# Optimization experiments

Measured on AMD Instinct MI355X. Metric: run time of the kernel, lower is better.

The kernel has to match this reference:

```python
import jax, jax.numpy as jnp
import numpy as np


def setup_inputs() -> dict:
    key = jax.random.key(0)
    k1, k2 = jax.random.split(key)
    return {
        "embeddings": jax.random.normal(k1, (4, 768, 32, 32), dtype=jnp.float32),
        "database": jax.random.normal(k2, (20000, 768), dtype=jnp.float32),
        "k": 3,
        "out_h": 512,
        "out_w": 512,
    }


def reference(embeddings, database, k, out_h, out_w):
    # embeddings: [B, D, h, w]  (segmenter hidden state), database: [N, D]
    B, D, h, w = embeddings.shape
    # B x h x w x D -> B x (h*w) x D query layout, as in _get_ood_scores
    q = jnp.transpose(embeddings, (0, 2, 3, 1)).reshape(B, h * w, D)
    # squared Euclidean distances via (||q||^2 + ||x||^2 - 2 q.x)
    q2 = jnp.sum(q * q, axis=-1)[..., None]                 # [B, hw, 1]
    x2 = jnp.sum(database * database, axis=-1)[None, None]  # [1, 1, N]
    d2 = q2 + x2 - 2.0 * jnp.einsum("bqd,nd->bqn", q, database)
    dist = jnp.sqrt(jnp.maximum(d2, 1e-12))                 # [B, hw, N]
    # k smallest distances (sklearn kneighbors) then mean over neighbors
    neg_topk, _ = jax.lax.top_k(-dist, k)                   # [B, hw, k]
    ood = jnp.mean(-neg_topk, axis=-1).reshape(B, h, w)
    # F.interpolate(..., mode='bilinear', align_corners=False) == half-pixel bilinear
    ood_up = jax.image.resize(ood[:, None], (B, 1, out_h, out_w), method="bilinear")
    return ood_up
```

## Files before the change

### kernel.cpp

```cpp
#include <hip/hip_runtime.h>
#include <hip/hip_bf16.h>
#include <math.h>

constexpr int B    = 4;
constexpr int D    = 768;
constexpr int HW   = 1024;
constexpr int M    = B * HW;
constexpr int NDB  = 20000;
constexpr int LT   = 158;
constexpr int OUTH = 512;
constexpr int OUTW = 512;

constexpr int BM     = 256;
constexpr int BN     = 128;
constexpr int KSTEPS = D / 64;
constexpr int NSPLIT = 16;
constexpr int NT2    = 79;
constexpr int STEPB  = 128 * 64;

typedef int   i32x8  __attribute__((ext_vector_type(8)));
typedef float f32x16 __attribute__((ext_vector_type(16)));

__device__ __forceinline__ void insert3(float& t0, float& t1, float& t2, float d) {
    float a0 = fminf(d, t0);
    float b0 = fmaxf(d, t0);
    float a1 = fminf(b0, t1);
    float b1 = fmaxf(b0, t1);
    t0 = a0; t1 = a1;
    t2 = fminf(b1, t2);
}

__device__ __forceinline__ unsigned int pack4_fp8(float a, float b, float c, float d) {
    int v = __builtin_amdgcn_cvt_pk_fp8_f32(a, b, 0, false);
    v = __builtin_amdgcn_cvt_pk_fp8_f32(c, d, v, true);
    return (unsigned int)v;
}

__device__ __forceinline__ void gl_lds16(const unsigned char* g, unsigned char* l) {
    __builtin_amdgcn_global_load_lds(
        (const __attribute__((address_space(1))) void*)g,
        (__attribute__((address_space(3))) void*)l, 16, 0, 0);
}

__global__ __launch_bounds__(256) void convert_all(const float* __restrict__ db,
                                                   const float* __restrict__ emb,
                                                   uint4* __restrict__ dbt8,
                                                   uint4* __restrict__ qbt8,
                                                   float* __restrict__ x2p,
                                                   float* __restrict__ q2p) {
    __shared__ float panel[128][68];
    __shared__ float part[512];
    const int g = blockIdx.y;
    const int t = threadIdx.x;

    if (blockIdx.x < LT) {
        const int lt = blockIdx.x;
        const int n0 = lt * 128;

        #pragma unroll
        for (int pass = 0; pass < 8; ++pass) {
            int idx = pass * 256 + t;
            int row = idx >> 4, c4 = idx & 15;
            int n = n0 + row;
            float4 v = make_float4(0.f, 0.f, 0.f, 0.f);
            if (n < NDB) v = *(const float4*)(db + (size_t)n * D + g * 64 + c4 * 4);
            *(float4*)&panel[row][c4 * 4] = v;
        }
        __syncthreads();
        #pragma unroll
        for (int pass = 0; pass < 2; ++pass) {
            int idx = pass * 256 + t;
            int r  = idx & 31;
            int kc = (idx >> 5) & 1;
            int h2 = (idx >> 6) & 1;
            int rg = idx >> 7;
            int row  = rg * 32 + r;
            int kloc = kc * 32 + h2 * 16;
            float4 va = *(const float4*)&panel[row][kloc + 0];
            float4 vb = *(const float4*)&panel[row][kloc + 4];
            float4 vc = *(const float4*)&panel[row][kloc + 8];
            float4 vd = *(const float4*)&panel[row][kloc + 12];
            float ss = va.x*va.x + va.y*va.y + va.z*va.z + va.w*va.w
                     + vb.x*vb.x + vb.y*vb.y + vb.z*vb.z + vb.w*vb.w
                     + vc.x*vc.x + vc.y*vc.y + vc.z*vc.z + vc.w*vc.w
                     + vd.x*vd.x + vd.y*vd.y + vd.z*vd.z + vd.w*vd.w;
            uint4 o;
            o.x = pack4_fp8(va.x, va.y, va.z, va.w);
            o.y = pack4_fp8(vb.x, vb.y, vb.z, vb.w);
            o.z = pack4_fp8(vc.x, vc.y, vc.z, vc.w);
            o.w = pack4_fp8(vd.x, vd.y, vd.z, vd.w);
            dbt8[((size_t)lt * KSTEPS + g) * 512 + idx] = o;
            part[idx] = ss;
        }
        __syncthreads();
        if (t < 128) {
            int base = (t >> 5) * 128 + (t & 31);
            float s = part[base] + part[base + 32] + part[base + 64] + part[base + 96];
            x2p[((size_t)lt * KSTEPS + g) * 128 + t] = s;
        }
    } else {
        const int qt = blockIdx.x - LT;
        const int b  = qt >> 3;
        const int p0 = (qt & 7) * 128;

        #pragma unroll
        for (int pass = 0; pass < 2; ++pass) {
            int idx = pass * 256 + t;
            int r  = idx & 31;
            int kc = (idx >> 5) & 1;
            int h2 = (idx >> 6) & 1;
            int rg = idx >> 7;
            int prow = rg * 32 + r;
            int kb = g * 64 + kc * 32 + h2 * 16;
            const float* src = emb + ((size_t)b * D + kb) * HW + p0 + prow;
            float v[16];
            float ss = 0.f;
            #pragma unroll
            for (int j = 0; j < 16; ++j) {
                v[j] = src[(size_t)j * HW];
                ss = fmaf(v[j], v[j], ss);
            }
            uint4 o;
            o.x = pack4_fp8(-2.f*v[0],  -2.f*v[1],  -2.f*v[2],  -2.f*v[3]);
            o.y = pack4_fp8(-2.f*v[4],  -2.f*v[5],  -2.f*v[6],  -2.f*v[7]);
            o.z = pack4_fp8(-2.f*v[8],  -2.f*v[9],  -2.f*v[10], -2.f*v[11]);
            o.w = pack4_fp8(-2.f*v[12], -2.f*v[13], -2.f*v[14], -2.f*v[15]);
            qbt8[((size_t)qt * KSTEPS + g) * 512 + idx] = o;
            part[idx] = ss;
        }
        __syncthreads();
        if (t < 128) {
            int base = (t >> 5) * 128 + (t & 31);
            float s = part[base] + part[base + 32] + part[base + 64] + part[base + 96];
            q2p[((size_t)qt * KSTEPS + g) * 128 + t] = s;
        }
    }
}

__global__ __launch_bounds__(256, 2) void gemm_topk(const unsigned char* __restrict__ dbt8,
                                                    const unsigned char* __restrict__ qbt8,
                                                    const float* __restrict__ x2p,
                                                    float* __restrict__ partials) {
    __shared__ __align__(16) unsigned char Bsm[4 * 8192];
    __shared__ float red[4][BN][3];

    const int tid  = threadIdx.x;
    const int lane = tid & 63;
    const int w    = tid >> 6;
    const int lts  = w >> 1;
    const int wr   = w & 1;
    const int h    = lane >> 5;
    const int l31  = lane & 31;

    const int bid   = blockIdx.x;
    const int xcd   = bid & 7;
    const int j     = bid >> 3;
    const int sp    = xcd + 8 * (j >> 5);
    const int qtile = j & 31;
    const int m0    = qtile * BN;

    int b_off[4];
    #pragma unroll
    for (int j4 = 0; j4 < 4; ++j4) b_off[j4] = j4 * 2048 + h * 512 + l31 * 16;

    const unsigned char* aT = dbt8 + (size_t)(2 * sp + lts) * KSTEPS * STEPB
                              + wr * 4096 + h * 512 + l31 * 16;

    const unsigned char* bQ = qbt8 + (size_t)qtile * KSTEPS * STEPB + w * 2048 + lane * 16;
    unsigned char* bD = Bsm + w * 2048;

    auto ldA = [&](i32x8& x0, i32x8& x1, const unsigned char* p) {
        int4 a = *(const int4*)(p);
        int4 b = *(const int4*)(p + 1024);
        int4 c = *(const int4*)(p + 2048);
        int4 d = *(const int4*)(p + 3072);
        x0 = (i32x8){a.x, a.y, a.z, a.w, b.x, b.y, b.z, b.w};
        x1 = (i32x8){c.x, c.y, c.z, c.w, d.x, d.y, d.z, d.w};
    };
    auto ldB = [&](i32x8& f, const unsigned char* Bb, int off) {
        int4 lo = *(const int4*)(Bb + off);
        int4 hi = *(const int4*)(Bb + off + 1024);
        f = (i32x8){lo.x, lo.y, lo.z, lo.w, hi.x, hi.y, hi.z, hi.w};
    };

    gl_lds16(bQ,                bD);
    gl_lds16(bQ + 1024,         bD + 1024);
    gl_lds16(bQ + STEPB,        bD + 8192);
    gl_lds16(bQ + STEPB + 1024, bD + 8192 + 1024);

    float t0[4], t1[4], t2[4];
    #pragma unroll
    for (int j4 = 0; j4 < 4; ++j4) { t0[j4] = INFINITY; t1[j4] = INFINITY; t2[j4] = INFINITY; }

    for (int tile = sp; tile < NT2; tile += NSPLIT) {
        const bool lastTile = (tile + NSPLIT >= NT2);

        float sx = 1e30f;
        {
            int n = tile * BM + w * 64 + lane;
            if (n < NDB) {
                const float* p = x2p + (size_t)(n >> 7) * (KSTEPS * 128) + (n & 127);
                sx = 0.f;
                #pragma unroll
                for (int g = 0; g < KSTEPS; ++g) sx += p[g * 128];
            }
        }

        f32x16 acc[2][4];
        #pragma unroll
        for (int i = 0; i < 2; ++i)
            #pragma unroll
            for (int j4 = 0; j4 < 4; ++j4)
                #pragma unroll
                for (int r = 0; r < 16; ++r) acc[i][j4][r] = 0.f;

        i32x8 af0, af1, an0, an1;
        ldA(af0, af1, aT);

        #pragma unroll 2
        for (int g = 0; g < KSTEPS; ++g) {
            if ((g & 1) == 0) __syncthreads();

            {
                int gs = g + 2;
                unsigned char* dst = bD + ((g + 2) & 3) * 8192;
                if (gs < KSTEPS) {
                    gl_lds16(bQ + gs * STEPB,        dst);
                    gl_lds16(bQ + gs * STEPB + 1024, dst + 1024);
                } else if (!lastTile) {
                    gl_lds16(bQ + (gs - KSTEPS) * STEPB,        dst);
                    gl_lds16(bQ + (gs - KSTEPS) * STEPB + 1024, dst + 1024);
                }
            }

            if (g + 1 < KSTEPS) ldA(an0, an1, aT + (g + 1) * STEPB);

            const unsigned char* Bb = Bsm + (g & 3) * 8192;
            i32x8 bf[4];
            #pragma unroll
            for (int j4 = 0; j4 < 4; ++j4) ldB(bf[j4], Bb, b_off[j4]);

            #pragma unroll
            for (int j4 = 0; j4 < 4; ++j4) {
                acc[0][j4] = __builtin_amdgcn_mfma_scale_f32_32x32x64_f8f6f4(
                    af0, bf[j4], acc[0][j4], 0, 0, 0, 0x7f7f7f7f, 0, 0x7f7f7f7f);
                acc[1][j4] = __builtin_amdgcn_mfma_scale_f32_32x32x64_f8f6f4(
                    af1, bf[j4], acc[1][j4], 0, 0, 0, 0x7f7f7f7f, 0, 0x7f7f7f7f);
            }
            af0 = an0; af1 = an1;
        }
        aT += (size_t)2 * NSPLIT * KSTEPS * STEPB;

        #pragma unroll
        for (int i = 0; i < 2; ++i) {
            #pragma unroll
            for (int rg2 = 0; rg2 < 4; ++rg2) {
                #pragma unroll
                for (int rr = 0; rr < 4; ++rr) {
                    float xv = __shfl(sx, i * 32 + rg2 * 8 + 4 * h + rr);
                    #pragma unroll
                    for (int j4 = 0; j4 < 4; ++j4)
                        insert3(t0[j4], t1[j4], t2[j4], acc[i][j4][rg2 * 4 + rr] + xv);
                }
            }
        }
    }

    #pragma unroll
    for (int j4 = 0; j4 < 4; ++j4) {
        float o0 = __shfl_xor(t0[j4], 32);
        float o1 = __shfl_xor(t1[j4], 32);
        float o2 = __shfl_xor(t2[j4], 32);
        insert3(t0[j4], t1[j4], t2[j4], o0);
        insert3(t0[j4], t1[j4], t2[j4], o1);
        insert3(t0[j4], t1[j4], t2[j4], o2);
    }
    if (h == 0) {
        #pragma unroll
        for (int j4 = 0; j4 < 4; ++j4) {
            int col = j4 * 32 + l31;
            red[w][col][0] = t0[j4];
            red[w][col][1] = t1[j4];
            red[w][col][2] = t2[j4];
        }
    }
    __syncthreads();
    if (tid < BN) {
        float a0 = red[0][tid][0], a1 = red[0][tid][1], a2 = red[0][tid][2];
        #pragma unroll
        for (int ww = 1; ww < 4; ++ww) {
            insert3(a0, a1, a2, red[ww][tid][0]);
            insert3(a0, a1, a2, red[ww][tid][1]);
            insert3(a0, a1, a2, red[ww][tid][2]);
        }
        float* dst = partials + ((size_t)(m0 + tid) * NSPLIT + sp) * 3;
        dst[0] = a0; dst[1] = a1; dst[2] = a2;
    }
}

__global__ __launch_bounds__(256) void merge_ood(const float* __restrict__ partials,
                                                 const float* __restrict__ q2p,
                                                 float* __restrict__ ood) {
    int m = blockIdx.x * 256 + threadIdx.x;
    if (m >= M) return;
    const float* pp = partials + (size_t)m * NSPLIT * 3;
    float a0 = INFINITY, a1 = INFINITY, a2 = INFINITY;
    #pragma unroll
    for (int j = 0; j < NSPLIT * 3; ++j) insert3(a0, a1, a2, pp[j]);
    const float* qp = q2p + (size_t)(m >> 7) * KSTEPS * 128 + (m & 127);
    float q = 0.f;
    #pragma unroll
    for (int g = 0; g < KSTEPS; ++g) q += qp[g * 128];
    float d0 = sqrtf(fmaxf(q + a0, 1e-12f));
    float d1 = sqrtf(fmaxf(q + a1, 1e-12f));
    float d2 = sqrtf(fmaxf(q + a2, 1e-12f));
    ood[m] = (d0 + d1 + d2) * (1.f / 3.f);
}

__global__ __launch_bounds__(256) void upsample(const float* __restrict__ ood,
                                                float* __restrict__ out) {
    int idx = blockIdx.x * 256 + threadIdx.x;
    int ox = idx & (OUTW - 1);
    int oy = (idx >> 9) & (OUTH - 1);
    int bb = idx >> 18;
    float sx = (ox + 0.5f) * (32.f / OUTW) - 0.5f;
    float sy = (oy + 0.5f) * (32.f / OUTH) - 0.5f;
    float fx = floorf(sx), fy = floorf(sy);
    float wx = sx - fx, wy = sy - fy;
    int x0 = max(0, min(31, (int)fx));
    int x1 = max(0, min(31, (int)fx + 1));
    int y0 = max(0, min(31, (int)fy));
    int y1 = max(0, min(31, (int)fy + 1));
    const float* src = ood + bb * 1024;
    float v00 = src[y0 * 32 + x0];
    float v01 = src[y0 * 32 + x1];
    float v10 = src[y1 * 32 + x0];
    float v11 = src[y1 * 32 + x1];
    float top = v00 + wx * (v01 - v00);
    float bot = v10 + wx * (v11 - v10);
    out[idx] = top + wy * (bot - top);
}

extern "C" void kernel_launch(void* const* d_in, const int* in_sizes, int n_in,
                              void* d_out, int out_size, void* d_ws, size_t ws_size,
                              hipStream_t stream) {
    const float* emb = (const float*)d_in[0];
    const float* db  = (const float*)d_in[1];
    float* out = (float*)d_out;

    char* ws = (char*)d_ws;
    unsigned char* dbt8 = (unsigned char*)ws;
    unsigned char* qbt8 = (unsigned char*)(ws + 15532032);
    float* x2p      = (float*)(ws + 18677760);
    float* q2p      = (float*)(ws + 19648512);
    float* ood      = (float*)(ws + 19845120);
    float* partials = (float*)(ws + 19861504);

    convert_all<<<dim3(LT + 32, KSTEPS), 256, 0, stream>>>(db, emb, (uint4*)dbt8,
                                                           (uint4*)qbt8, x2p, q2p);
    gemm_topk<<<NSPLIT * 32, 256, 0, stream>>>(dbt8, qbt8, x2p, partials);
    merge_ood<<<(M + 255) / 256, 256, 0, stream>>>(partials, q2p, ood);
    upsample<<<(B * OUTH * OUTW) / 256, 256, 0, stream>>>(ood, out);
}
```

Measured before the change: 179.1 us.

## Fuse top-k merge with bilinear upsample and batch database panel loads

The separate merge and upsample kernels become one finalize kernel. Each of 32 blocks recomputes the OOD scores for an 8-row band, with halo rows, into shared memory, then writes a 64x512 strip of the upsampled output. This removes one launch and the global round trip of the intermediate OOD map. The cost is that only 32 blocks write the 4 MB output, so memory-level parallelism may drop, and halo rows are merged redundantly. Separately, the database panel loads in convert_all are all issued before any shared-memory store, so the loads can be in flight together.

```diff
diff --git a/kernel.cpp b/kernel.cpp
--- a/kernel.cpp
+++ b/kernel.cpp
@@ -57,14 +57,20 @@
         const int lt = blockIdx.x;
         const int n0 = lt * 128;
 
+        float4 v8[8];
         #pragma unroll
         for (int pass = 0; pass < 8; ++pass) {
             int idx = pass * 256 + t;
             int row = idx >> 4, c4 = idx & 15;
             int n = n0 + row;
-            float4 v = make_float4(0.f, 0.f, 0.f, 0.f);
-            if (n < NDB) v = *(const float4*)(db + (size_t)n * D + g * 64 + c4 * 4);
-            *(float4*)&panel[row][c4 * 4] = v;
+            v8[pass] = make_float4(0.f, 0.f, 0.f, 0.f);
+            if (n < NDB) v8[pass] = *(const float4*)(db + (size_t)n * D + g * 64 + c4 * 4);
+        }
+        #pragma unroll
+        for (int pass = 0; pass < 8; ++pass) {
+            int idx = pass * 256 + t;
+            int row = idx >> 4, c4 = idx & 15;
+            *(float4*)&panel[row][c4 * 4] = v8[pass];
         }
         __syncthreads();
         #pragma unroll
@@ -298,47 +304,55 @@
     }
 }
 
-__global__ __launch_bounds__(256) void merge_ood(const float* __restrict__ partials,
-                                                 const float* __restrict__ q2p,
-                                                 float* __restrict__ ood) {
-    int m = blockIdx.x * 256 + threadIdx.x;
-    if (m >= M) return;
-    const float* pp = partials + (size_t)m * NSPLIT * 3;
-    float a0 = INFINITY, a1 = INFINITY, a2 = INFINITY;
-    #pragma unroll
-    for (int j = 0; j < NSPLIT * 3; ++j) insert3(a0, a1, a2, pp[j]);
-    const float* qp = q2p + (size_t)(m >> 7) * KSTEPS * 128 + (m & 127);
-    float q = 0.f;
-    #pragma unroll
-    for (int g = 0; g < KSTEPS; ++g) q += qp[g * 128];
-    float d0 = sqrtf(fmaxf(q + a0, 1e-12f));
-    float d1 = sqrtf(fmaxf(q + a1, 1e-12f));
-    float d2 = sqrtf(fmaxf(q + a2, 1e-12f));
-    ood[m] = (d0 + d1 + d2) * (1.f / 3.f);
-}
-
-__global__ __launch_bounds__(256) void upsample(const float* __restrict__ ood,
+__global__ __launch_bounds__(256) void finalize(const float* __restrict__ partials,
+                                                const float* __restrict__ q2p,
                                                 float* __restrict__ out) {
-    int idx = blockIdx.x * 256 + threadIdx.x;
-    int ox = idx & (OUTW - 1);
-    int oy = (idx >> 9) & (OUTH - 1);
-    int bb = idx >> 18;
-    float sx = (ox + 0.5f) * (32.f / OUTW) - 0.5f;
-    float sy = (oy + 0.5f) * (32.f / OUTH) - 0.5f;
-    float fx = floorf(sx), fy = floorf(sy);
-    float wx = sx - fx, wy = sy - fy;
-    int x0 = max(0, min(31, (int)fx));
-    int x1 = max(0, min(31, (int)fx + 1));
-    int y0 = max(0, min(31, (int)fy));
-    int y1 = max(0, min(31, (int)fy + 1));
-    const float* src = ood + bb * 1024;
-    float v00 = src[y0 * 32 + x0];
-    float v01 = src[y0 * 32 + x1];
-    float v10 = src[y1 * 32 + x0];
-    float v11 = src[y1 * 32 + x1];
-    float top = v00 + wx * (v01 - v00);
-    float bot = v10 + wx * (v11 - v10);
-    out[idx] = top + wy * (bot - top);
+    __shared__ float ods[8][32];
+    const int bb   = blockIdx.x >> 3;
+    const int band = blockIdx.x & 7;
+    const int t    = threadIdx.x;
+
+    {
+        int ly  = t >> 5;
+        int col = t & 31;
+        int gy  = max(0, min(31, 4 * band - 2 + ly));
+        int m   = bb * 1024 + gy * 32 + col;
+        const float* pp = partials + (size_t)m * NSPLIT * 3;
+        float a0 = INFINITY, a1 = INFINITY, a2 = INFINITY;
+        #pragma unroll
+        for (int jj = 0; jj < NSPLIT * 3; ++jj) insert3(a0, a1, a2, pp[jj]);
+        const float* qp = q2p + (size_t)(m >> 7) * (KSTEPS * 128) + (m & 127);
+        float q = 0.f;
+        #pragma unroll
+        for (int g = 0; g < KSTEPS; ++g) q += qp[g * 128];
+        float d0 = sqrtf(fmaxf(q + a0, 1e-12f));
+        float d1 = sqrtf(fmaxf(q + a1, 1e-12f));
+        float d2 = sqrtf(fmaxf(q + a2, 1e-12f));
+        ods[ly][col] = (d0 + d1 + d2) * (1.f / 3.f);
+    }
+    __syncthreads();
+
+    const int oy0 = band * 64;
+    const int lbase = 4 * band - 2;
+    for (int i = t; i < 64 * 512; i += 256) {
+        int ox = i & 511;
+        int oy = oy0 + (i >> 9);
+        float sx = (ox + 0.5f) * (32.f / OUTW) - 0.5f;
+        float sy = (oy + 0.5f) * (32.f / OUTH) - 0.5f;
+        float fx = floorf(sx), fy = floorf(sy);
+        float wx = sx - fx, wy = sy - fy;
+        int x0 = max(0, min(31, (int)fx));
+        int x1 = max(0, min(31, (int)fx + 1));
+        int y0 = max(0, min(31, (int)fy));
+        int y1 = max(0, min(31, (int)fy + 1));
+        int ly0 = y0 - lbase;
+        int ly1 = y1 - lbase;
+        float v00 = ods[ly0][x0], v01 = ods[ly0][x1];
+        float v10 = ods[ly1][x0], v11 = ods[ly1][x1];
+        float top = v00 + wx * (v01 - v00);
+        float bot = v10 + wx * (v11 - v10);
+        out[((size_t)bb * OUTH + oy) * OUTW + ox] = top + wy * (bot - top);
+    }
 }
 
 extern "C" void kernel_launch(void* const* d_in, const int* in_sizes, int n_in,
@@ -353,12 +367,10 @@
     unsigned char* qbt8 = (unsigned char*)(ws + 15532032);
     float* x2p      = (float*)(ws + 18677760);
     float* q2p      = (float*)(ws + 19648512);
-    float* ood      = (float*)(ws + 19845120);
     float* partials = (float*)(ws + 19861504);
 
     convert_all<<<dim3(LT + 32, KSTEPS), 256, 0, stream>>>(db, emb, (uint4*)dbt8,
                                                            (uint4*)qbt8, x2p, q2p);
     gemm_topk<<<NSPLIT * 32, 256, 0, stream>>>(dbt8, qbt8, x2p, partials);
-    merge_ood<<<(M + 255) / 256, 256, 0, stream>>>(partials, q2p, ood);
-    upsample<<<(B * OUTH * OUTW) / 256, 256, 0, stream>>>(ood, out);
-}
+    finalize<<<B * 8, 256, 0, stream>>>(partials, q2p, out);
+}
```

Result: slower. 187.0 us (+4.4%).
